# Performance work log

Measured on AMD Instinct MI355X. Metric: run time of the kernel, lower is better.

Reference implementation:

```python
import jax, jax.numpy as jnp
import numpy as np


def setup_inputs() -> dict:
    key = jax.random.key(0)
    x = jax.random.normal(key, (8, 2048, 3), dtype=jnp.float32)
    return {"x": x, "k": 16}


def reference(x, k):
    b, n, d = x.shape
    xf = x.reshape(b * n, d)                      # flatten across batch, as in the torch module
    sq = jnp.sum(xf * xf, axis=1, keepdims=True)  # [BN, 1]
    pair = 2.0 * (xf @ xf.T) - sq - sq.T          # [BN, BN] = -dist^2
    # torch topk(largest=False) on pair == largest of (-pair) == largest squared distance
    neg_vals, idx = jax.lax.top_k(-pair, k + 1)   # [BN, k+1]
    dists = -neg_vals
    dists = dists[:, 1:].reshape(b, n, k)
    idx = idx[:, 1:].reshape(b, n, k)
    return dists, idx
```

## Files before the change

kernel.cpp:

```cpp
#include <hip/hip_runtime.h>
#include <stdint.h>

#define BN       16384
#define NTILES   256
#define NB       64
#define KOUT     16
#define MARGIN   0.01f

typedef float v2f __attribute__((ext_vector_type(2)));
union F4 { float4 f4; v2f p[2]; float f[4]; };

#define WS_TAB    0
#define WS_IDX    (WS_TAB + BN * 16)
#define WS_BND    (WS_IDX + BN * 4)
#define WS_HIST   (WS_BND + NTILES * 8)
#define WS_HMAX   (WS_HIST + 64 * NB * 4)
#define WS_CBASE  (WS_HMAX + 64 * NB * 4)

__device__ __forceinline__ unsigned key_u(unsigned u) {
    return u ^ ((unsigned)((int)u >> 31) | 0x80000000u);
}
__device__ __forceinline__ unsigned wshr1(unsigned v, unsigned oldv) {
    return (unsigned)__builtin_amdgcn_update_dpp((int)oldv, (int)v, 0x138 ,
                                                 0xF, 0xF, false);
}
#define RL16(T) __uint_as_float((unsigned)__builtin_amdgcn_readlane(__float_as_int(T), 16))

__device__ __forceinline__ float sq_of(float gx, float gy, float gz) {
    return __fadd_rn(__fadd_rn(__fmul_rn(gx, gx), __fmul_rn(gy, gy)), __fmul_rn(gz, gz));
}
__device__ __forceinline__ int bucket_of(float sq) {
    const float rho = __fsqrt_rn(sq);
    int b = (int)(64.0f * (1.0f - rho * 0.2f));
    return (b < 0) ? 0 : ((b > 63) ? 63 : b);
}

#define DRAIN(m, p, jvec, T, J)                                                     \
    while (m) {                                                                     \
        const int b_ = (int)__builtin_ctzll(m);                                     \
        m &= m - 1;                                                                 \
        const float pc_ = __uint_as_float(                                          \
            (unsigned)__builtin_amdgcn_readlane(__float_as_int(p), b_));            \
        const unsigned jc_ = (unsigned)__builtin_amdgcn_readlane((int)(jvec), b_);  \
        const float Tup_ =                                                          \
            __uint_as_float(wshr1(__float_as_uint(T), 0xFF800000u ));       \
        const unsigned Jup_ = wshr1((J), 0u);                                       \
        const bool lt_ = (pc_ < Tup_) || ((pc_ == Tup_) && (jc_ < Jup_));           \
        const float Tn_ = lt_ ? Tup_ : pc_;                                         \
        const unsigned Jn_ = lt_ ? Jup_ : jc_;                                      \
        const bool sel_ = (pc_ < (T)) || ((pc_ == (T)) && (jc_ < (J)));             \
        (T) = sel_ ? Tn_ : (T);                                                     \
        (J) = sel_ ? Jn_ : (J);                                                     \
    }

#define EVALC(c, d2)                                                                \
    asm("v_pk_mul_f32 %0, %1, %2 op_sel:[0,0] op_sel_hi:[0,1]"                      \
        : "=v"(d2) : "v"((c).p[0]), "v"(c0A));                                      \
    asm("v_pk_fma_f32 %0, %1, %2, %0 op_sel:[1,0,0] op_sel_hi:[1,1,1]"              \
        : "+v"(d2) : "v"((c).p[0]), "v"(c1A));                                      \
    asm("v_pk_fma_f32 %0, %1, %2, %0 op_sel:[0,0,0] op_sel_hi:[0,1,1]"              \
        : "+v"(d2) : "v"((c).p[1]), "v"(c2A));                                      \
    asm("v_pk_add_f32 %0, %0, %1" : "+v"(d2) : "v"(nsq01));                         \
    asm("v_pk_add_f32 %0, %0, %1 op_sel:[0,1] op_sel_hi:[1,1]"                      \
        : "+v"(d2) : "v"((c).p[1]));

#define TILE_AT(t)                                                                  \
    F4 c; c.f4 = tab[(t) * 64 + lane];                                              \
    const unsigned jvec = idxarr[(t) * 64 + lane];                                  \
    v2f d2; EVALC(c, d2)

#define PROCESS_LOADED()                                                            \
    do {                                                                            \
        uint64_t m0 = __ballot(d2[0] <= fF0);                                       \
        uint64_t m1 = __ballot(d2[1] <= fF1);                                       \
        if (m0 | m1) {                                                              \
            const float p0 = d2[0], p1 = d2[1];                                     \
            DRAIN(m0, p0, jvec, T0, J0)                                             \
            DRAIN(m1, p1, jvec, T1, J1)                                             \
            fF0 = RL16(T0); thr0 = __fsub_rn(-fF0, MARGIN);                         \
            fF1 = RL16(T1); thr1 = __fsub_rn(-fF1, MARGIN);                         \
        }                                                                           \
    } while (0)

__device__ __forceinline__ void presort64(float p, unsigned j, int lane, double* sw,
                                          float& T, unsigned& J) {
    const double dm = (double)key_u(__float_as_uint(p)) * 16384.0 + (double)j;
    sw[lane] = dm;
    unsigned rank = 0;
    const char* sb = (const char*)sw;
    unsigned off = (unsigned)lane * 8u;
#pragma unroll 7
    for (int s = 1; s < 64; ++s) {
        off = (off + 8u) & 511u;
        const double dn = *(const double*)(sb + off);
        rank += (dn < dm) ? 1u : 0u;
    }
    sw[rank] = __longlong_as_double(
        (long long)(((unsigned long long)j << 32) | __float_as_uint(p)));
    const unsigned long long v = (unsigned long long)__double_as_longlong(sw[lane]);
    T = __uint_as_float((unsigned)(v & 0xFFFFFFFFull));
    J = (unsigned)(v >> 32);
}

__global__ __launch_bounds__(256) void k_hist(const float* __restrict__ x,
                                              unsigned* __restrict__ hist,
                                              unsigned* __restrict__ hmax) {
    __shared__ unsigned h[NB], m[NB];
    const int tid = threadIdx.x;
    if (tid < NB) { h[tid] = 0u; m[tid] = 0u; }
    __syncthreads();
    const int i = blockIdx.x * 256 + tid;
    const float sq = sq_of(x[3 * i], x[3 * i + 1], x[3 * i + 2]);
    const int b = bucket_of(sq);
    atomicAdd(&h[b], 1u);
    atomicMax(&m[b], __float_as_uint(sq));
    __syncthreads();
    if (tid < NB) {
        hist[blockIdx.x * NB + tid] = h[tid];
        hmax[blockIdx.x * NB + tid] = m[tid];
    }
}

__global__ __launch_bounds__(256) void k_mid(const unsigned* __restrict__ hist,
                                             const unsigned* __restrict__ hmax,
                                             unsigned* __restrict__ cbase,
                                             float2* __restrict__ bnd) {
    __shared__ unsigned tot[NB], basev[NB + 1], sfx[NB];
    const int tid = threadIdx.x;
    if (tid < NB) {
        unsigned s = 0, mx = 0;
        for (int g = 0; g < 64; ++g) {
            s += hist[g * NB + tid];
            const unsigned w = hmax[g * NB + tid];
            mx = (w > mx) ? w : mx;
        }
        tot[tid] = s;
        sfx[tid] = mx;
    }
    __syncthreads();
    if (tid == 0) {
        unsigned s = 0;
        for (int b = 0; b < NB; ++b) { basev[b] = s; s += tot[b]; }
        basev[NB] = s;
        unsigned M = 0;
        for (int b = NB - 1; b >= 0; --b) { const unsigned w = sfx[b]; M = (w > M) ? w : M; sfx[b] = M; }
    }
    __syncthreads();
    if (tid < NB) {
        unsigned s = basev[tid];
        for (int g = 0; g < 64; ++g) {
            cbase[g * NB + tid] = s;
            s += hist[g * NB + tid];
        }
    }
    {
        const unsigned pos = (unsigned)tid * 64u;
        int b = 0;
        for (int bb = 0; bb < NB; ++bb)
            if (basev[bb] <= pos && pos < basev[bb + 1]) b = bb;
        const float B = __uint_as_float(sfx[b]);
        const float sqB_up = __uint_as_float(__float_as_uint(__fsqrt_rn(B)) + 2u);
        bnd[tid] = make_float2(B, sqB_up);
    }
}

__global__ __launch_bounds__(256) void k_scatter(const float* __restrict__ x,
                                                 const unsigned* __restrict__ cbase,
                                                 float4* __restrict__ tab,
                                                 unsigned* __restrict__ idxarr) {
    __shared__ unsigned c[NB];
    const int tid = threadIdx.x;
    if (tid < NB) c[tid] = 0u;
    __syncthreads();
    const int i = blockIdx.x * 256 + tid;
    const float gx = x[3 * i], gy = x[3 * i + 1], gz = x[3 * i + 2];
    const float sq = sq_of(gx, gy, gz);
    const int b = bucket_of(sq);
    const unsigned r = atomicAdd(&c[b], 1u);
    const unsigned pos = cbase[blockIdx.x * NB + b] + r;
    tab[pos] = make_float4(gx, gy, gz, -sq);
    idxarr[pos] = (unsigned)i;
}

__global__ __launch_bounds__(256) void knn_far_kernel(
    const float* __restrict__ x, const float4* __restrict__ tab,
    const unsigned* __restrict__ idxarr, const float2* __restrict__ bnd,
    float* __restrict__ out_d, float* __restrict__ out_i) {
    __shared__ double swall[4 * 64];
    const int tid  = threadIdx.x;
    const int lane = tid & 63;
    const int wid  = tid >> 6;
    double* sw = swall + wid * 64;
    const int q0 = (blockIdx.x * 4 + wid) * 2;
    const int q1 = q0 + 1;

    const float a0 = x[3 * q0], a1 = x[3 * q0 + 1], a2 = x[3 * q0 + 2];
    const float b0 = x[3 * q1], b1 = x[3 * q1 + 1], b2 = x[3 * q1 + 2];
    const float sq0 = sq_of(a0, a1, a2), sq1 = sq_of(b0, b1, b2);
    const v2f nsq01 = {-sq0, -sq1};
    const v2f c0A = {2.0f * a0, 2.0f * b0};
    const v2f c1A = {2.0f * a1, 2.0f * b1};
    const v2f c2A = {2.0f * a2, 2.0f * b2};
    const float twor0 = 2.0f * __uint_as_float(__float_as_uint(__fsqrt_rn(sq0)) + 2u);
    const float twor1 = 2.0f * __uint_as_float(__float_as_uint(__fsqrt_rn(sq1)) + 2u);

    float T0, T1; unsigned J0, J1;
    float fF0, fF1, thr0, thr1;

    {
        TILE_AT(0)
        presort64(d2[0], jvec, lane, sw, T0, J0);
        presort64(d2[1], jvec, lane, sw, T1, J1);
        fF0 = RL16(T0); thr0 = __fsub_rn(-fF0, MARGIN);
        fF1 = RL16(T1); thr1 = __fsub_rn(-fF1, MARGIN);
    }
#pragma unroll
    for (int t = 1; t < 4; ++t) {
        TILE_AT(t)
        PROCESS_LOADED();
    }
    for (int t = 4; t < NTILES; ++t) {
        const float2 bd = bnd[t];
        const float u0 = __builtin_fmaf(twor0, bd.y, __fadd_rn(sq0, bd.x));
        const float u1 = __builtin_fmaf(twor1, bd.y, __fadd_rn(sq1, bd.x));
        if (u0 < thr0 && u1 < thr1) break;
        TILE_AT(t)
        PROCESS_LOADED();
    }

    if (lane >= 1 && lane <= KOUT) {
        const int r = lane - 1;
        out_d[q0 * KOUT + r] = T0;
        out_i[q0 * KOUT + r] = (float)J0;
        out_d[q1 * KOUT + r] = T1;
        out_i[q1 * KOUT + r] = (float)J1;
    }
}

extern "C" void kernel_launch(void* const* d_in, const int* in_sizes, int n_in,
                              void* d_out, int out_size, void* d_ws, size_t ws_size,
                              hipStream_t stream) {
    const float* x = (const float*)d_in[0];
    char* ws = (char*)d_ws;
    float4*   tab    = (float4*)(ws + WS_TAB);
    unsigned* idxarr = (unsigned*)(ws + WS_IDX);
    float2*   bnd    = (float2*)(ws + WS_BND);
    unsigned* hist   = (unsigned*)(ws + WS_HIST);
    unsigned* hmax   = (unsigned*)(ws + WS_HMAX);
    unsigned* cbase  = (unsigned*)(ws + WS_CBASE);
    float* out_d = (float*)d_out;
    float* out_i = out_d + (size_t)BN * KOUT;

    hipLaunchKernelGGL(k_hist,    dim3(64), dim3(256), 0, stream, x, hist, hmax);
    hipLaunchKernelGGL(k_mid,     dim3(1),  dim3(256), 0, stream, hist, hmax, cbase, bnd);
    hipLaunchKernelGGL(k_scatter, dim3(64), dim3(256), 0, stream, x, cbase, tab, idxarr);
    hipLaunchKernelGGL(knn_far_kernel, dim3(BN / 8), dim3(256), 0, stream,
                       x, tab, idxarr, bnd, out_d, out_i);
}
```

Measured before the change: 83.38 us.

## Fuse mid and scatter kernels, precompute early-exit tile, use 16-bit indices

Merges the single-block prefix kernel and the scatter kernel into one 64-block prep kernel. Each block computes its own column base with a wave shuffle scan, and block 0 writes the tile bounds. The main kernel now reads queries in sorted order from the table and stores indices as 16-bit values. It also replaces the per-tile scalar bound check with a wave-wide ballot that computes the cutoff tile once and recomputes it only when the threshold changes. This removes one launch and the serial prefix work, and cuts index bandwidth and the per-iteration bound loads. It relies on indices fitting in 16 bits and adds ballot work on each threshold update.

```diff
diff --git a/kernel.cpp b/kernel.cpp
--- a/kernel.cpp
+++ b/kernel.cpp
@@ -15,7 +15,6 @@
 #define WS_BND    (WS_IDX + BN * 4)
 #define WS_HIST   (WS_BND + NTILES * 8)
 #define WS_HMAX   (WS_HIST + 64 * NB * 4)
-#define WS_CBASE  (WS_HMAX + 64 * NB * 4)
 
 __device__ __forceinline__ unsigned key_u(unsigned u) {
     return u ^ ((unsigned)((int)u >> 31) | 0x80000000u);
@@ -66,7 +65,7 @@
 
 #define TILE_AT(t)                                                                  \
     F4 c; c.f4 = tab[(t) * 64 + lane];                                              \
-    const unsigned jvec = idxarr[(t) * 64 + lane];                                  \
+    const unsigned jvec = (unsigned)idx16[(t) * 64 + lane];                         \
     v2f d2; EVALC(c, d2)
 
 #define PROCESS_LOADED()                                                            \
@@ -74,12 +73,26 @@
         uint64_t m0 = __ballot(d2[0] <= fF0);                                       \
         uint64_t m1 = __ballot(d2[1] <= fF1);                                       \
         if (m0 | m1) {                                                              \
-            const float p0 = d2[0], p1 = d2[1];                                     \
-            DRAIN(m0, p0, jvec, T0, J0)                                             \
-            DRAIN(m1, p1, jvec, T1, J1)                                             \
+            const float p0v = d2[0], p1v = d2[1];                                   \
+            DRAIN(m0, p0v, jvec, T0, J0)                                            \
+            DRAIN(m1, p1v, jvec, T1, J1)                                            \
             fF0 = RL16(T0); thr0 = __fsub_rn(-fF0, MARGIN);                         \
             fF1 = RL16(T1); thr1 = __fsub_rn(-fF1, MARGIN);                         \
         }                                                                           \
+    } while (0)
+
+#define CERTM(bd)                                                                    \
+    __ballot((__builtin_fmaf(twor0, (bd)[1], __fadd_rn(sq0, (bd)[0])) < thr0) &&     \
+             (__builtin_fmaf(twor1, (bd)[1], __fadd_rn(sq1, (bd)[0])) < thr1))
+
+#define COMPUTE_TSTAR()                                                              \
+    do {                                                                             \
+        uint64_t mm;                                                                 \
+        if ((mm = CERTM(bdA)))        ts = (int)__builtin_ctzll(mm);                 \
+        else if ((mm = CERTM(bdB)))   ts = 64  + (int)__builtin_ctzll(mm);           \
+        else if ((mm = CERTM(bdC)))   ts = 128 + (int)__builtin_ctzll(mm);           \
+        else if ((mm = CERTM(bdD)))   ts = 192 + (int)__builtin_ctzll(mm);           \
+        else                          ts = NTILES;                                   \
     } while (0)
 
 __device__ __forceinline__ void presort64(float p, unsigned j, int lane, double* sw,
@@ -121,88 +134,95 @@
     }
 }
 
-__global__ __launch_bounds__(256) void k_mid(const unsigned* __restrict__ hist,
-                                             const unsigned* __restrict__ hmax,
-                                             unsigned* __restrict__ cbase,
-                                             float2* __restrict__ bnd) {
-    __shared__ unsigned tot[NB], basev[NB + 1], sfx[NB];
+__global__ __launch_bounds__(256) void k_prep(const float* __restrict__ x,
+                                              const unsigned* __restrict__ hist,
+                                              const unsigned* __restrict__ hmax,
+                                              float4* __restrict__ tab,
+                                              unsigned short* __restrict__ idx16,
+                                              float2* __restrict__ bnd) {
+    __shared__ unsigned colbase[NB], cur[NB], basev[NB + 1], mxv[NB], sfxs[NB];
     const int tid = threadIdx.x;
+    const int blk = blockIdx.x;
     if (tid < NB) {
-        unsigned s = 0, mx = 0;
+        unsigned tot = 0u, part = 0u, mx = 0u;
+#pragma unroll 8
         for (int g = 0; g < 64; ++g) {
-            s += hist[g * NB + tid];
+            const unsigned h = hist[g * NB + tid];
+            tot += h;
+            part += (g < blk) ? h : 0u;
             const unsigned w = hmax[g * NB + tid];
             mx = (w > mx) ? w : mx;
         }
-        tot[tid] = s;
-        sfx[tid] = mx;
+        unsigned v = tot;
+#pragma unroll
+        for (int s = 1; s < 64; s <<= 1) {
+            const unsigned n = (unsigned)__shfl_up((int)v, (unsigned)s, 64);
+            v += (tid >= s) ? n : 0u;
+        }
+        basev[tid] = v - tot;
+        if (tid == NB - 1) basev[NB] = v;
+        colbase[tid] = (v - tot) + part;
+        cur[tid] = 0u;
+        mxv[tid] = mx;
     }
     __syncthreads();
-    if (tid == 0) {
-        unsigned s = 0;
-        for (int b = 0; b < NB; ++b) { basev[b] = s; s += tot[b]; }
-        basev[NB] = s;
-        unsigned M = 0;
-        for (int b = NB - 1; b >= 0; --b) { const unsigned w = sfx[b]; M = (w > M) ? w : M; sfx[b] = M; }
-    }
-    __syncthreads();
-    if (tid < NB) {
-        unsigned s = basev[tid];
-        for (int g = 0; g < 64; ++g) {
-            cbase[g * NB + tid] = s;
-            s += hist[g * NB + tid];
-        }
-    }
-    {
-        const unsigned pos = (unsigned)tid * 64u;
-        int b = 0;
-        for (int bb = 0; bb < NB; ++bb)
-            if (basev[bb] <= pos && pos < basev[bb + 1]) b = bb;
-        const float B = __uint_as_float(sfx[b]);
-        const float sqB_up = __uint_as_float(__float_as_uint(__fsqrt_rn(B)) + 2u);
-        bnd[tid] = make_float2(B, sqB_up);
-    }
-}
-
-__global__ __launch_bounds__(256) void k_scatter(const float* __restrict__ x,
-                                                 const unsigned* __restrict__ cbase,
-                                                 float4* __restrict__ tab,
-                                                 unsigned* __restrict__ idxarr) {
-    __shared__ unsigned c[NB];
-    const int tid = threadIdx.x;
-    if (tid < NB) c[tid] = 0u;
-    __syncthreads();
-    const int i = blockIdx.x * 256 + tid;
+    const int i = blk * 256 + tid;
     const float gx = x[3 * i], gy = x[3 * i + 1], gz = x[3 * i + 2];
     const float sq = sq_of(gx, gy, gz);
     const int b = bucket_of(sq);
-    const unsigned r = atomicAdd(&c[b], 1u);
-    const unsigned pos = cbase[blockIdx.x * NB + b] + r;
+    const unsigned r = atomicAdd(&cur[b], 1u);
+    const unsigned pos = colbase[b] + r;
     tab[pos] = make_float4(gx, gy, gz, -sq);
-    idxarr[pos] = (unsigned)i;
+    idx16[pos] = (unsigned short)i;
+
+    if (blk == 0) {
+        if (tid == 0) {
+            unsigned M = 0u;
+            for (int b2 = NB - 1; b2 >= 0; --b2) {
+                const unsigned w = mxv[b2];
+                M = (w > M) ? w : M;
+                sfxs[b2] = M;
+            }
+        }
+        __syncthreads();
+        const unsigned posb = (unsigned)tid * 64u;
+        int bb = 0;
+        for (int t2 = 0; t2 < NB; ++t2)
+            if (basev[t2] <= posb && posb < basev[t2 + 1]) bb = t2;
+        const float B = __uint_as_float(sfxs[bb]);
+        const float sqB_up = __uint_as_float(__float_as_uint(__fsqrt_rn(B)) + 2u);
+        bnd[tid] = make_float2(B, sqB_up);
+    }
 }
 
 __global__ __launch_bounds__(256) void knn_far_kernel(
-    const float* __restrict__ x, const float4* __restrict__ tab,
-    const unsigned* __restrict__ idxarr, const float2* __restrict__ bnd,
-    float* __restrict__ out_d, float* __restrict__ out_i) {
+    const float4* __restrict__ tab, const unsigned short* __restrict__ idx16,
+    const float2* __restrict__ bnd, float* __restrict__ out_d, float* __restrict__ out_i) {
     __shared__ double swall[4 * 64];
     const int tid  = threadIdx.x;
     const int lane = tid & 63;
     const int wid  = tid >> 6;
     double* sw = swall + wid * 64;
-    const int q0 = (blockIdx.x * 4 + wid) * 2;
-    const int q1 = q0 + 1;
-
-    const float a0 = x[3 * q0], a1 = x[3 * q0 + 1], a2 = x[3 * q0 + 2];
-    const float b0 = x[3 * q1], b1 = x[3 * q1 + 1], b2 = x[3 * q1 + 2];
-    const float sq0 = sq_of(a0, a1, a2), sq1 = sq_of(b0, b1, b2);
-    const v2f nsq01 = {-sq0, -sq1};
-    const v2f c0A = {2.0f * a0, 2.0f * b0};
-    const v2f c1A = {2.0f * a1, 2.0f * b1};
-    const v2f c2A = {2.0f * a2, 2.0f * b2};
+    const int p0 = (blockIdx.x * 4 + wid) * 2;
+    const int p1 = p0 + 1;
+
+    F4 qa; qa.f4 = tab[p0];
+    F4 qb; qb.f4 = tab[p1];
+    const unsigned q0 = (unsigned)idx16[p0];
+    const unsigned q1 = (unsigned)idx16[p1];
+    const float sq0 = -qa.f[3], sq1 = -qb.f[3];
+    const v2f nsq01 = {qa.f[3], qb.f[3]};
+    const v2f c0A = {2.0f * qa.f[0], 2.0f * qb.f[0]};
+    const v2f c1A = {2.0f * qa.f[1], 2.0f * qb.f[1]};
+    const v2f c2A = {2.0f * qa.f[2], 2.0f * qb.f[2]};
     const float twor0 = 2.0f * __uint_as_float(__float_as_uint(__fsqrt_rn(sq0)) + 2u);
     const float twor1 = 2.0f * __uint_as_float(__float_as_uint(__fsqrt_rn(sq1)) + 2u);
+
+    const v2f* bndv = (const v2f*)bnd;
+    const v2f bdA = bndv[lane];
+    const v2f bdB = bndv[64 + lane];
+    const v2f bdC = bndv[128 + lane];
+    const v2f bdD = bndv[192 + lane];
 
     float T0, T1; unsigned J0, J1;
     float fF0, fF1, thr0, thr1;
@@ -219,13 +239,21 @@
         TILE_AT(t)
         PROCESS_LOADED();
     }
-    for (int t = 4; t < NTILES; ++t) {
-        const float2 bd = bnd[t];
-        const float u0 = __builtin_fmaf(twor0, bd.y, __fadd_rn(sq0, bd.x));
-        const float u1 = __builtin_fmaf(twor1, bd.y, __fadd_rn(sq1, bd.x));
-        if (u0 < thr0 && u1 < thr1) break;
+
+    int ts;
+    COMPUTE_TSTAR();
+    for (int t = 4; t < ts; ++t) {
         TILE_AT(t)
-        PROCESS_LOADED();
+        uint64_t m0 = __ballot(d2[0] <= fF0);
+        uint64_t m1 = __ballot(d2[1] <= fF1);
+        if (m0 | m1) {
+            const float p0v = d2[0], p1v = d2[1];
+            DRAIN(m0, p0v, jvec, T0, J0)
+            DRAIN(m1, p1v, jvec, T1, J1)
+            fF0 = RL16(T0); thr0 = __fsub_rn(-fF0, MARGIN);
+            fF1 = RL16(T1); thr1 = __fsub_rn(-fF1, MARGIN);
+            COMPUTE_TSTAR();
+        }
     }
 
     if (lane >= 1 && lane <= KOUT) {
@@ -242,18 +270,17 @@
                               hipStream_t stream) {
     const float* x = (const float*)d_in[0];
     char* ws = (char*)d_ws;
-    float4*   tab    = (float4*)(ws + WS_TAB);
-    unsigned* idxarr = (unsigned*)(ws + WS_IDX);
-    float2*   bnd    = (float2*)(ws + WS_BND);
-    unsigned* hist   = (unsigned*)(ws + WS_HIST);
-    unsigned* hmax   = (unsigned*)(ws + WS_HMAX);
-    unsigned* cbase  = (unsigned*)(ws + WS_CBASE);
+    float4*         tab   = (float4*)(ws + WS_TAB);
+    unsigned short* idx16 = (unsigned short*)(ws + WS_IDX);
+    float2*         bnd   = (float2*)(ws + WS_BND);
+    unsigned*       hist  = (unsigned*)(ws + WS_HIST);
+    unsigned*       hmax  = (unsigned*)(ws + WS_HMAX);
     float* out_d = (float*)d_out;
     float* out_i = out_d + (size_t)BN * KOUT;
 
-    hipLaunchKernelGGL(k_hist,    dim3(64), dim3(256), 0, stream, x, hist, hmax);
-    hipLaunchKernelGGL(k_mid,     dim3(1),  dim3(256), 0, stream, hist, hmax, cbase, bnd);
-    hipLaunchKernelGGL(k_scatter, dim3(64), dim3(256), 0, stream, x, cbase, tab, idxarr);
+    hipLaunchKernelGGL(k_hist, dim3(64), dim3(256), 0, stream, x, hist, hmax);
+    hipLaunchKernelGGL(k_prep, dim3(64), dim3(256), 0, stream, x, hist, hmax,
+                       tab, idx16, bnd);
     hipLaunchKernelGGL(knn_far_kernel, dim3(BN / 8), dim3(256), 0, stream,
-                       x, tab, idxarr, bnd, out_d, out_i);
-}
+                       tab, idx16, bnd, out_d, out_i);
+}
```

Measured after the change: 77.21 us. 7.4% less time.
